# Optimization experiments

Hardware: AMD Instinct MI355X
Metric: run time of the kernel (lower is better)

The kernel has to match this reference:

```python
import jax, jax.numpy as jnp
from jax import lax
import numpy as np

GZ = 15.0   # grid extent (float, from gz=15.0)
G = 15      # grid cells per axis


def _disty(p):
    # p: [B, N, 3] points in [0, GZ). 12 features per point:
    # offsets to cell center / lower corner / upper corner (9) + their euclidean norms (3)
    c = jnp.floor(jnp.clip(p, 0.0, GZ - 1e-4))
    off_c = p - (c + 0.5)
    off_l = p - c
    off_u = p - (c + 1.0)
    norms = jnp.stack([jnp.sqrt((o * o).sum(-1)) for o in (off_c, off_l, off_u)], axis=-1)
    return jnp.concatenate([off_c, off_l, off_u, norms], axis=-1)  # [B, N, 12]


def _mlp(x, W1, b1, W2, b2, W3, b3):
    h = jax.nn.elu(x @ W1 + b1)
    h = jax.nn.elu(h @ W2 + b2)
    return h @ W3 + b3  # [B, N, 4]


def _agg(feats, p):
    # scatter-max per-point features into the [G,G,G] grid of each scene
    B, N, C = feats.shape
    cell = jnp.floor(jnp.clip(p, 0.0, GZ - 1e-4)).astype(jnp.int32)  # [B, N, 3]
    flat = (cell[..., 0] * G + cell[..., 1]) * G + cell[..., 2]
    flat = flat + (jnp.arange(B, dtype=jnp.int32) * (G ** 3))[:, None]
    grid = jnp.zeros((B * G ** 3, C), feats.dtype)
    grid = grid.at[flat.reshape(-1)].max(feats.reshape(-1, C))
    return grid.reshape(B, G, G, G, C).transpose(0, 4, 1, 2, 3)  # [B, 4, G, G, G]


def _conv_bn_elu(x, w, b, g, beta, stride):
    y = lax.conv_general_dilated(x, w, (stride,) * 3, [(2, 2)] * 3,
                                 dimension_numbers=('NCDHW', 'OIDHW', 'NCDHW'))
    y = y + b[None, :, None, None, None]
    # BatchNorm3d, training mode (batch statistics), eps=1e-5
    m = y.mean((0, 2, 3, 4), keepdims=True)
    v = ((y - m) ** 2).mean((0, 2, 3, 4), keepdims=True)
    y = (y - m) * lax.rsqrt(v + 1e-5)
    y = y * g[None, :, None, None, None] + beta[None, :, None, None, None]
    return jax.nn.elu(y)


def setup_inputs():
    key = jax.random.key(0)
    ks = jax.random.split(key, 16)
    B, N = 4, 300000
    pts = lambda k: jax.random.uniform(k, (B, N, 3), jnp.float32, 0.0, GZ)
    lin = lambda k, i, o: (jax.random.normal(k, (i, o), jnp.float32) / np.sqrt(i)).astype(jnp.float32)
    inp = {
        'goals': pts(ks[0]), 'inputs': pts(ks[1]), 'backgrounds': pts(ks[2]),
        'W1': lin(ks[3], 12, 16), 'b1': jnp.zeros((16,), jnp.float32),
        'W2': lin(ks[4], 16, 16), 'b2': jnp.zeros((16,), jnp.float32),
        'W3': lin(ks[5], 16, 4),  'b3': jnp.zeros((4,), jnp.float32),
        'conv1_w': (jax.random.normal(ks[6], (8, 12, 5, 5, 5), jnp.float32) / np.sqrt(12 * 125)).astype(jnp.float32),
        'conv1_b': jnp.zeros((8,), jnp.float32),
        'bn1_g': jnp.ones((8,), jnp.float32), 'bn1_b': jnp.zeros((8,), jnp.float32),
        'convs_w': (jax.random.normal(ks[7], (6, 8, 8, 5, 5, 5), jnp.float32) / np.sqrt(8 * 125)).astype(jnp.float32),
        'convs_b': jnp.zeros((6, 8), jnp.float32),
        'bns_g': jnp.ones((6, 8), jnp.float32), 'bns_b': jnp.zeros((6, 8), jnp.float32),
    }
    return inp


def reference(goals, inputs, backgrounds, W1, b1, W2, b2, W3, b3,
              conv1_w, conv1_b, bn1_g, bn1_b, convs_w, convs_b, bns_g, bns_b):
    def encode(p):
        return _agg(_mlp(_disty(p), W1, b1, W2, b2, W3, b3), p)

    scenes = jnp.concatenate([encode(inputs), encode(goals), encode(backgrounds)], axis=1)  # [B,12,G,G,G]
    x = _conv_bn_elu(scenes, conv1_w, conv1_b, bn1_g, bn1_b, 2)  # [B,8,8,8,8]
    for i in range(6):
        x = _conv_bn_elu(x, convs_w[i], convs_b[i], bns_g[i], bns_b[i], 1)
    return x
```

## Files before the change

kernel.cpp:

```cpp
#include <hip/hip_runtime.h>
#include <math.h>

#define B 4
#define NPTS 300000
#define G 15
#define G3 3375
#define PAIR_FLOATS (4*G3)
#define SCENE_FLOATS (B*12*G3)

typedef float v2f __attribute__((ext_vector_type(2)));

__device__ __forceinline__ float eluf(float v) {
    return v > 0.0f ? v : __expf(v) - 1.0f;
}

__global__ __launch_bounds__(256)
void mlp_kernel(const float* __restrict__ P0,
                const float* __restrict__ P1,
                const float* __restrict__ P2,
                const float* __restrict__ W1, const float* __restrict__ b1,
                const float* __restrict__ W2, const float* __restrict__ b2,
                const float* __restrict__ W3, const float* __restrict__ b3,
                float4* __restrict__ vals, unsigned short* __restrict__ cells,
                float* __restrict__ stats,
                int s0, int m)
{
    if (blockIdx.x == 0 && blockIdx.y == 0 && blockIdx.z == 0 && threadIdx.x < 128)
        stats[threadIdx.x] = 0.0f;

    int b   = blockIdx.y;
    int set = blockIdx.z;
    int i   = blockIdx.x * 256 + threadIdx.x;
    if (i >= m) return;
    const float* P = (set == 0) ? P0 : ((set == 1) ? P1 : P2);

    const float* p = P + ((size_t)b * NPTS + (size_t)(s0 + i)) * 3;
    float px = p[0], py = p[1], pz = p[2];

    const float HI = 14.9999f;
    float cx = floorf(fminf(fmaxf(px, 0.0f), HI));
    float cy = floorf(fminf(fmaxf(py, 0.0f), HI));
    float cz = floorf(fminf(fmaxf(pz, 0.0f), HI));

    float x[12];
    x[0] = px - (cx + 0.5f); x[1] = py - (cy + 0.5f); x[2] = pz - (cz + 0.5f);
    x[3] = px - cx;          x[4] = py - cy;          x[5] = pz - cz;
    x[6] = px - (cx + 1.0f); x[7] = py - (cy + 1.0f); x[8] = pz - (cz + 1.0f);
    x[9]  = sqrtf(x[0]*x[0] + x[1]*x[1] + x[2]*x[2]);
    x[10] = sqrtf(x[3]*x[3] + x[4]*x[4] + x[5]*x[5]);
    x[11] = sqrtf(x[6]*x[6] + x[7]*x[7] + x[8]*x[8]);

    const v2f* W1v = (const v2f*)W1;
    const v2f* W2v = (const v2f*)W2;
    const v2f* W3v = (const v2f*)W3;
    const v2f* b1v = (const v2f*)b1;
    const v2f* b2v = (const v2f*)b2;
    const v2f* b3v = (const v2f*)b3;

    float h1[16];
#pragma unroll
    for (int j2 = 0; j2 < 8; ++j2) {
        v2f s = b1v[j2];
#pragma unroll
        for (int k = 0; k < 12; ++k) {
            v2f xb; xb.x = x[k]; xb.y = x[k];
            s = xb * W1v[k * 8 + j2] + s;
        }
        h1[2*j2]   = eluf(s.x);
        h1[2*j2+1] = eluf(s.y);
    }
    float h2[16];
#pragma unroll
    for (int j2 = 0; j2 < 8; ++j2) {
        v2f s = b2v[j2];
#pragma unroll
        for (int k = 0; k < 16; ++k) {
            v2f xb; xb.x = h1[k]; xb.y = h1[k];
            s = xb * W2v[k * 8 + j2] + s;
        }
        h2[2*j2]   = eluf(s.x);
        h2[2*j2+1] = eluf(s.y);
    }
    v2f o01 = b3v[0], o23 = b3v[1];
#pragma unroll
    for (int k = 0; k < 16; ++k) {
        v2f xb; xb.x = h2[k]; xb.y = h2[k];
        o01 = xb * W3v[k * 2 + 0] + o01;
        o23 = xb * W3v[k * 2 + 1] + o23;
    }

    int cell = (((int)cx) * G + (int)cy) * G + (int)cz;
    int pair = b * 3 + set;
    vals [(size_t)pair * m + i] = make_float4(o01.x, o01.y, o23.x, o23.y);
    cells[(size_t)pair * m + i] = (unsigned short)cell;
}

__global__ __launch_bounds__(512)
void scatter_kernel(const float4* __restrict__ vals,
                    const unsigned short* __restrict__ cells,
                    float* __restrict__ scenesR, int K, int m, int carry)
{
    __shared__ unsigned sg[PAIR_FLOATS];

    int rep = blockIdx.x;
    int b   = blockIdx.y;
    int set = blockIdx.z;
    int pair = b * 3 + set;
    float* myrep = scenesR + ((size_t)pair * K + rep) * PAIR_FLOATS;

    if (carry) {
        for (int i = threadIdx.x; i < PAIR_FLOATS; i += 512)
            sg[i] = __float_as_uint(myrep[i]);
    } else {
        for (int i = threadIdx.x; i < PAIR_FLOATS; i += 512)
            sg[i] = 0u;
    }
    __syncthreads();

    int chunk = (m + K - 1) / K;
    int start = rep * chunk;
    int end   = min(m, start + chunk);
    const float4*         v = vals  + (size_t)pair * m;
    const unsigned short* c = cells + (size_t)pair * m;

    for (int i = start + (int)threadIdx.x; i < end; i += 512) {
        float4 o = v[i];
        int cell = c[i];
        if (o.x > 0.0f) atomicMax(&sg[          cell], __float_as_uint(o.x));
        if (o.y > 0.0f) atomicMax(&sg[    G3 + cell], __float_as_uint(o.y));
        if (o.z > 0.0f) atomicMax(&sg[2 * G3 + cell], __float_as_uint(o.z));
        if (o.w > 0.0f) atomicMax(&sg[3 * G3 + cell], __float_as_uint(o.w));
    }
    __syncthreads();

    for (int i = threadIdx.x; i < PAIR_FLOATS; i += 512)
        myrep[i] = __uint_as_float(sg[i]);
}

__global__ __launch_bounds__(256)
void reduce_kernel(const float* __restrict__ scenesR, float* __restrict__ scenes,
                   int K)
{
    int t = blockIdx.x * 256 + threadIdx.x;
    if (t >= SCENE_FLOATS) return;
    int pair = t / PAIR_FLOATS;
    int j    = t - pair * PAIR_FLOATS;
    const float* src = scenesR + (size_t)pair * K * PAIR_FLOATS + j;
    float mx = 0.0f;
    for (int r = 0; r < K; ++r)
        mx = fmaxf(mx, src[(size_t)r * PAIR_FLOATS]);
    scenes[t] = mx;
}

__global__ __launch_bounds__(768)
void conv1_kernel(const float* __restrict__ scenes,
                  const float* __restrict__ w,
                  const float* __restrict__ bias,
                  float* __restrict__ y, float* __restrict__ stats)
{
    __shared__ float sred[768];
    int bx = blockIdx.x;
    int od = bx & 7, co = (bx >> 3) & 7, b = bx >> 6;
    int tid = threadIdx.x;
    int ow = tid & 7, oh = (tid >> 3) & 7, ci = tid >> 6;

    const float* sc = scenes + (size_t)(b * 12 + ci) * G3;
    const float* wc = w + (size_t)(co * 12 + ci) * 125;
    float s = 0.0f;
#pragma unroll
    for (int kd = 0; kd < 5; ++kd) {
        int id = od * 2 - 2 + kd;
        if ((unsigned)id >= (unsigned)G) continue;
#pragma unroll
        for (int kh = 0; kh < 5; ++kh) {
            int ih = oh * 2 - 2 + kh;
            bool hok = (unsigned)ih < (unsigned)G;
#pragma unroll
            for (int kw = 0; kw < 5; ++kw) {
                int iw = ow * 2 - 2 + kw;
                if (hok && (unsigned)iw < (unsigned)G)
                    s = fmaf(sc[(id * G + ih) * G + iw], wc[kd*25 + kh*5 + kw], s);
            }
        }
    }
    sred[tid] = s;
    __syncthreads();
    if (tid < 64) {
        float tot = bias[co];
#pragma unroll
        for (int g2 = 0; g2 < 12; ++g2) tot += sred[g2 * 64 + tid];
        y[(size_t)(b * 8 + co) * 512 + od * 64 + tid] = tot;
        float sum = tot, sq = tot * tot;
#pragma unroll
        for (int o = 32; o > 0; o >>= 1) {
            sum += __shfl_down(sum, o, 64);
            sq  += __shfl_down(sq,  o, 64);
        }
        if (tid == 0) { atomicAdd(&stats[co], sum); atomicAdd(&stats[8 + co], sq); }
    }
}

__global__ __launch_bounds__(512)
void conv_s_kernel(const float* __restrict__ yin,
                   const float* __restrict__ w,
                   const float* __restrict__ bias,
                   const float* __restrict__ g, const float* __restrict__ bet,
                   const float* __restrict__ stats_in,
                   float* __restrict__ yout, float* __restrict__ stats_out)
{
    __shared__ float slab[8 * 5 * 144];
    __shared__ float sstat[16], sscale[8], sshift[8];
    __shared__ float sred[512];

    int bx = blockIdx.x;
    int od = bx & 7, co = (bx >> 3) & 7, b = bx >> 6;
    int tid = threadIdx.x;

    float raw[8];
#pragma unroll
    for (int k = 0; k < 8; ++k) {
        int r = k * 512 + tid;
        raw[k] = yin[((size_t)(b * 8) << 9) + r];
    }

    if (tid < 16) sstat[tid] = stats_in[tid];
    for (int i = tid; i < 5760; i += 512) slab[i] = 0.0f;
    __syncthreads();

    if (tid < 8) {
        float S = sstat[tid], Q = sstat[8 + tid];
        float m  = S * (1.0f / 2048.0f);
        float vv = Q * (1.0f / 2048.0f) - m * m;
        float rs = rsqrtf(vv + 1e-5f);
        float sc = g[tid] * rs;
        sscale[tid] = sc;
        sshift[tid] = bet[tid] - m * sc;
    }
    __syncthreads();

#pragma unroll
    for (int k = 0; k < 8; ++k) {
        int r  = k * 512 + tid;
        int ci = r >> 9, rem = r & 511;
        int id = rem >> 6, ih = (rem >> 3) & 7, iw = rem & 7;
        int kd = id - od + 2;
        if ((unsigned)kd < 5u) {
            float t = fmaf(raw[k], sscale[ci], sshift[ci]);
            slab[ci * 720 + kd * 144 + (ih + 2) * 12 + (iw + 2)] =
                t > 0.0f ? t : __expf(t) - 1.0f;
        }
    }
    __syncthreads();

    int ow = tid & 7, oh = (tid >> 3) & 7, ci = tid >> 6;
    const float* sl = slab + ci * 720;
    const float* wc = w + (size_t)(co * 8 + ci) * 125;
    float s = 0.0f;
#pragma unroll
    for (int kd = 0; kd < 5; ++kd) {
#pragma unroll
        for (int kh = 0; kh < 5; ++kh) {
            const float* row = sl + kd * 144 + (oh + kh) * 12 + ow;
            const float* wr = wc + kd * 25 + kh * 5;
#pragma unroll
            for (int kw = 0; kw < 5; ++kw) s = fmaf(row[kw], wr[kw], s);
        }
    }
    sred[tid] = s;
    __syncthreads();
    if (tid < 64) {
        float tot = bias[co];
#pragma unroll
        for (int g2 = 0; g2 < 8; ++g2) tot += sred[g2 * 64 + tid];
        yout[(size_t)(b * 8 + co) * 512 + od * 64 + tid] = tot;
        float sum = tot, sq = tot * tot;
#pragma unroll
        for (int o = 32; o > 0; o >>= 1) {
            sum += __shfl_down(sum, o, 64);
            sq  += __shfl_down(sq,  o, 64);
        }
        if (tid == 0) { atomicAdd(&stats_out[co], sum); atomicAdd(&stats_out[8 + co], sq); }
    }
}

__global__ __launch_bounds__(256)
void bn_final_kernel(const float* __restrict__ yin,
                     const float* __restrict__ g, const float* __restrict__ bet,
                     const float* __restrict__ stats_in, float* __restrict__ outp)
{
    int i = blockIdx.x * 256 + threadIdx.x;
    float v = yin[i];
    int c = (i >> 9) & 7;
    float S = stats_in[c], Q = stats_in[8 + c];
    float m  = S * (1.0f / 2048.0f);
    float vv = Q * (1.0f / 2048.0f) - m * m;
    float rs = rsqrtf(vv + 1e-5f);
    float sc = g[c] * rs;
    float sh = bet[c] - m * sc;
    float t = fmaf(v, sc, sh);
    outp[i] = t > 0.0f ? t : __expf(t) - 1.0f;
}

extern "C" void kernel_launch(void* const* d_in, const int* in_sizes, int n_in,
                              void* d_out, int out_size, void* d_ws, size_t ws_size,
                              hipStream_t stream)
{
    const float* goals       = (const float*)d_in[0];
    const float* inputs      = (const float*)d_in[1];
    const float* backgrounds = (const float*)d_in[2];
    const float* W1 = (const float*)d_in[3];
    const float* b1 = (const float*)d_in[4];
    const float* W2 = (const float*)d_in[5];
    const float* b2 = (const float*)d_in[6];
    const float* W3 = (const float*)d_in[7];
    const float* b3 = (const float*)d_in[8];
    const float* conv1_w = (const float*)d_in[9];
    const float* conv1_b = (const float*)d_in[10];
    const float* bn1_g   = (const float*)d_in[11];
    const float* bn1_b   = (const float*)d_in[12];
    const float* convs_w = (const float*)d_in[13];
    const float* convs_b = (const float*)d_in[14];
    const float* bns_g   = (const float*)d_in[15];
    const float* bns_b   = (const float*)d_in[16];

    long ws_floats = (long)(ws_size / 4);
    long fixed = SCENE_FLOATS + 2L * 16384 + 128;
    static const int plans[][2] = {
        {42,1},{42,2},{42,4},{24,4},{21,6},{16,8},{8,12},{4,16},{2,32},{1,64}};
    int K = 1, S = 64;
    for (int pi = 0; pi < 10; ++pi) {
        int pk = plans[pi][0], ps = plans[pi][1];
        long mseg = (NPTS + ps - 1) / ps;
        long need = 54L * mseg + (long)pk * SCENE_FLOATS + fixed;
        if (need <= ws_floats) { K = pk; S = ps; break; }
    }
    int Mseg = (NPTS + S - 1) / S;

    float*          wsp     = (float*)d_ws;
    float4*         vals    = (float4*)wsp;
    unsigned short* cells   = (unsigned short*)(wsp + 48L * Mseg);
    float*          scenesR = wsp + 54L * Mseg;
    float*          scenes  = scenesR + (size_t)K * SCENE_FLOATS;
    float*          yA      = scenes + SCENE_FLOATS;
    float*          yB      = yA + 16384;
    float*          stats   = yB + 16384;

    for (int s = 0; s < S; ++s) {
        int s0 = s * Mseg;
        int m  = min(Mseg, NPTS - s0);
        dim3 agrid((m + 255) / 256, B, 3);
        mlp_kernel<<<agrid, 256, 0, stream>>>(inputs, goals, backgrounds,
                                              W1, b1, W2, b2, W3, b3,
                                              vals, cells, stats, s0, m);
        dim3 bgrid(K, B, 3);
        scatter_kernel<<<bgrid, 512, 0, stream>>>(vals, cells, scenesR, K, m,
                                                  s > 0 ? 1 : 0);
    }

    reduce_kernel<<<(SCENE_FLOATS + 255) / 256, 256, 0, stream>>>(scenesR, scenes, K);

    conv1_kernel<<<256, 768, 0, stream>>>(scenes, conv1_w, conv1_b, yA, stats);

    const float* cur = yA;
    float* nxt = yB;
    for (int i = 0; i < 6; ++i) {
        const float* g   = (i == 0) ? bn1_g : (bns_g + (i - 1) * 8);
        const float* bet = (i == 0) ? bn1_b : (bns_b + (i - 1) * 8);
        conv_s_kernel<<<256, 512, 0, stream>>>(
            cur, convs_w + (size_t)i * 8000, convs_b + i * 8,
            g, bet, stats + i * 16, nxt, stats + (i + 1) * 16);
        const float* tmp = cur; cur = nxt; nxt = (float*)tmp;
    }

    bn_final_kernel<<<64, 256, 0, stream>>>(cur, bns_g + 5 * 8, bns_b + 5 * 8,
                                            stats + 6 * 16, (float*)d_out);
}
```

Baseline: 279.7 us.

## Merge scatter replicas with global atomicMax and fuse final BN into last conv

The per-replica scene buffers and the separate reduce kernel are removed. Each scatter block now merges its shared-memory grid directly into a single global scene buffer with atomicMax, and that buffer is zeroed inside the first MLP launch. The standalone BN/ELU epilogue kernel is folded into the last conv_s launch using a last-block-done counter with coherent loads. This cuts two kernel launches and the replica write/read traffic, but adds global atomic contention and depends on relaxed-atomic ordering for correctness.

```diff
diff --git a/kernel.cpp b/kernel.cpp
--- a/kernel.cpp
+++ b/kernel.cpp
@@ -7,11 +7,20 @@
 #define G3 3375
 #define PAIR_FLOATS (4*G3)
 #define SCENE_FLOATS (B*12*G3)
+#define RCHUNKS 42
 
 typedef float v2f __attribute__((ext_vector_type(2)));
 
 __device__ __forceinline__ float eluf(float v) {
     return v > 0.0f ? v : __expf(v) - 1.0f;
+}
+
+__device__ __forceinline__ float coh_load(const float* p) {
+    return __hip_atomic_fetch_add((float*)p, 0.0f, __ATOMIC_RELAXED,
+                                  __HIP_MEMORY_SCOPE_AGENT);
+}
+__device__ __forceinline__ void coh_store(float* p, float v) {
+    __hip_atomic_exchange(p, v, __ATOMIC_RELAXED, __HIP_MEMORY_SCOPE_AGENT);
 }
 
 __global__ __launch_bounds__(256)
@@ -22,11 +31,18 @@
                 const float* __restrict__ W2, const float* __restrict__ b2,
                 const float* __restrict__ W3, const float* __restrict__ b3,
                 float4* __restrict__ vals, unsigned short* __restrict__ cells,
-                float* __restrict__ stats,
+                float* __restrict__ stats, float* __restrict__ scenes,
                 int s0, int m)
 {
-    if (blockIdx.x == 0 && blockIdx.y == 0 && blockIdx.z == 0 && threadIdx.x < 128)
-        stats[threadIdx.x] = 0.0f;
+    if (s0 == 0) {
+        if (blockIdx.x == 0 && blockIdx.y == 0 && blockIdx.z == 0 &&
+            threadIdx.x < 128)
+            stats[threadIdx.x] = 0.0f;
+        if (blockIdx.y == 0 && blockIdx.z == 0) {
+            int t = blockIdx.x * 256 + threadIdx.x;
+            if (t < SCENE_FLOATS) scenes[t] = 0.0f;
+        }
+    }
 
     int b   = blockIdx.y;
     int set = blockIdx.z;
@@ -98,7 +114,7 @@
 __global__ __launch_bounds__(512)
 void scatter_kernel(const float4* __restrict__ vals,
                     const unsigned short* __restrict__ cells,
-                    float* __restrict__ scenesR, int K, int m, int carry)
+                    float* __restrict__ scenes, int m)
 {
     __shared__ unsigned sg[PAIR_FLOATS];
 
@@ -106,18 +122,11 @@
     int b   = blockIdx.y;
     int set = blockIdx.z;
     int pair = b * 3 + set;
-    float* myrep = scenesR + ((size_t)pair * K + rep) * PAIR_FLOATS;
-
-    if (carry) {
-        for (int i = threadIdx.x; i < PAIR_FLOATS; i += 512)
-            sg[i] = __float_as_uint(myrep[i]);
-    } else {
-        for (int i = threadIdx.x; i < PAIR_FLOATS; i += 512)
-            sg[i] = 0u;
-    }
-    __syncthreads();
-
-    int chunk = (m + K - 1) / K;
+
+    for (int i = threadIdx.x; i < PAIR_FLOATS; i += 512) sg[i] = 0u;
+    __syncthreads();
+
+    int chunk = (m + RCHUNKS - 1) / RCHUNKS;
     int start = rep * chunk;
     int end   = min(m, start + chunk);
     const float4*         v = vals  + (size_t)pair * m;
@@ -133,23 +142,11 @@
     }
     __syncthreads();
 
-    for (int i = threadIdx.x; i < PAIR_FLOATS; i += 512)
-        myrep[i] = __uint_as_float(sg[i]);
-}
-
-__global__ __launch_bounds__(256)
-void reduce_kernel(const float* __restrict__ scenesR, float* __restrict__ scenes,
-                   int K)
-{
-    int t = blockIdx.x * 256 + threadIdx.x;
-    if (t >= SCENE_FLOATS) return;
-    int pair = t / PAIR_FLOATS;
-    int j    = t - pair * PAIR_FLOATS;
-    const float* src = scenesR + (size_t)pair * K * PAIR_FLOATS + j;
-    float mx = 0.0f;
-    for (int r = 0; r < K; ++r)
-        mx = fmaxf(mx, src[(size_t)r * PAIR_FLOATS]);
-    scenes[t] = mx;
+    unsigned* dst = (unsigned*)scenes + (size_t)pair * PAIR_FLOATS;
+    for (int i = threadIdx.x; i < PAIR_FLOATS; i += 512) {
+        unsigned u = sg[i];
+        if (u) atomicMax(dst + i, u);
+    }
 }
 
 __global__ __launch_bounds__(768)
@@ -206,7 +203,10 @@
                    const float* __restrict__ bias,
                    const float* __restrict__ g, const float* __restrict__ bet,
                    const float* __restrict__ stats_in,
-                   float* __restrict__ yout, float* __restrict__ stats_out)
+                   float* __restrict__ yout, float* __restrict__ stats_out,
+                   const float* __restrict__ gN, const float* __restrict__ betN,
+                   unsigned* __restrict__ cnt, float* __restrict__ outp,
+                   int last)
 {
     __shared__ float slab[8 * 5 * 144];
     __shared__ float sstat[16], sscale[8], sshift[8];
@@ -272,7 +272,9 @@
         float tot = bias[co];
 #pragma unroll
         for (int g2 = 0; g2 < 8; ++g2) tot += sred[g2 * 64 + tid];
-        yout[(size_t)(b * 8 + co) * 512 + od * 64 + tid] = tot;
+        size_t oidx = ((size_t)(b * 8 + co) << 9) + od * 64 + tid;
+        if (last) coh_store(yout + oidx, tot);
+        else      yout[oidx] = tot;
         float sum = tot, sq = tot * tot;
 #pragma unroll
         for (int o = 32; o > 0; o >>= 1) {
@@ -281,24 +283,37 @@
         }
         if (tid == 0) { atomicAdd(&stats_out[co], sum); atomicAdd(&stats_out[8 + co], sq); }
     }
-}
-
-__global__ __launch_bounds__(256)
-void bn_final_kernel(const float* __restrict__ yin,
-                     const float* __restrict__ g, const float* __restrict__ bet,
-                     const float* __restrict__ stats_in, float* __restrict__ outp)
-{
-    int i = blockIdx.x * 256 + threadIdx.x;
-    float v = yin[i];
-    int c = (i >> 9) & 7;
-    float S = stats_in[c], Q = stats_in[8 + c];
-    float m  = S * (1.0f / 2048.0f);
-    float vv = Q * (1.0f / 2048.0f) - m * m;
-    float rs = rsqrtf(vv + 1e-5f);
-    float sc = g[c] * rs;
-    float sh = bet[c] - m * sc;
-    float t = fmaf(v, sc, sh);
-    outp[i] = t > 0.0f ? t : __expf(t) - 1.0f;
+
+    if (!last) return;
+
+    __syncthreads();
+    __shared__ unsigned amLast;
+    if (tid == 0) {
+        unsigned old = __hip_atomic_fetch_add(cnt, 1u, __ATOMIC_RELAXED,
+                                              __HIP_MEMORY_SCOPE_AGENT);
+        amLast = (old == 255u) ? 1u : 0u;
+    }
+    __syncthreads();
+    if (!amLast) return;
+
+    __shared__ float fsc[8], fsh[8];
+    if (tid < 8) {
+        float S = coh_load(stats_out + tid);
+        float Q = coh_load(stats_out + 8 + tid);
+        float mm = S * (1.0f / 2048.0f);
+        float vv = Q * (1.0f / 2048.0f) - mm * mm;
+        float rs = rsqrtf(vv + 1e-5f);
+        float sc2 = gN[tid] * rs;
+        fsc[tid] = sc2;
+        fsh[tid] = betN[tid] - mm * sc2;
+    }
+    __syncthreads();
+    for (int i2 = tid; i2 < 16384; i2 += 512) {
+        float v = coh_load(yout + i2);
+        int c = (i2 >> 9) & 7;
+        float t = fmaf(v, fsc[c], fsh[c]);
+        outp[i2] = t > 0.0f ? t : __expf(t) - 1.0f;
+    }
 }
 
 extern "C" void kernel_launch(void* const* d_in, const int* in_sizes, int n_in,
@@ -325,25 +340,21 @@
 
     long ws_floats = (long)(ws_size / 4);
     long fixed = SCENE_FLOATS + 2L * 16384 + 128;
-    static const int plans[][2] = {
-        {42,1},{42,2},{42,4},{24,4},{21,6},{16,8},{8,12},{4,16},{2,32},{1,64}};
-    int K = 1, S = 64;
-    for (int pi = 0; pi < 10; ++pi) {
-        int pk = plans[pi][0], ps = plans[pi][1];
+    int S = 64;
+    for (int ps = 1; ps <= 64; ps *= 2) {
         long mseg = (NPTS + ps - 1) / ps;
-        long need = 54L * mseg + (long)pk * SCENE_FLOATS + fixed;
-        if (need <= ws_floats) { K = pk; S = ps; break; }
+        if (54L * mseg + fixed <= ws_floats) { S = ps; break; }
     }
     int Mseg = (NPTS + S - 1) / S;
 
     float*          wsp     = (float*)d_ws;
     float4*         vals    = (float4*)wsp;
     unsigned short* cells   = (unsigned short*)(wsp + 48L * Mseg);
-    float*          scenesR = wsp + 54L * Mseg;
-    float*          scenes  = scenesR + (size_t)K * SCENE_FLOATS;
+    float*          scenes  = wsp + 54L * Mseg;
     float*          yA      = scenes + SCENE_FLOATS;
     float*          yB      = yA + 16384;
     float*          stats   = yB + 16384;
+    unsigned*       cnt     = (unsigned*)(stats + 116);
 
     for (int s = 0; s < S; ++s) {
         int s0 = s * Mseg;
@@ -351,13 +362,10 @@
         dim3 agrid((m + 255) / 256, B, 3);
         mlp_kernel<<<agrid, 256, 0, stream>>>(inputs, goals, backgrounds,
                                               W1, b1, W2, b2, W3, b3,
-                                              vals, cells, stats, s0, m);
-        dim3 bgrid(K, B, 3);
-        scatter_kernel<<<bgrid, 512, 0, stream>>>(vals, cells, scenesR, K, m,
-                                                  s > 0 ? 1 : 0);
-    }
-
-    reduce_kernel<<<(SCENE_FLOATS + 255) / 256, 256, 0, stream>>>(scenesR, scenes, K);
+                                              vals, cells, stats, scenes, s0, m);
+        dim3 bgrid(RCHUNKS, B, 3);
+        scatter_kernel<<<bgrid, 512, 0, stream>>>(vals, cells, scenes, m);
+    }
 
     conv1_kernel<<<256, 768, 0, stream>>>(scenes, conv1_w, conv1_b, yA, stats);
 
@@ -368,10 +376,9 @@
         const float* bet = (i == 0) ? bn1_b : (bns_b + (i - 1) * 8);
         conv_s_kernel<<<256, 512, 0, stream>>>(
             cur, convs_w + (size_t)i * 8000, convs_b + i * 8,
-            g, bet, stats + i * 16, nxt, stats + (i + 1) * 16);
+            g, bet, stats + i * 16, nxt, stats + (i + 1) * 16,
+            bns_g + 5 * 8, bns_b + 5 * 8, cnt, (float*)d_out,
+            (i == 5) ? 1 : 0);
         const float* tmp = cur; cur = nxt; nxt = (float*)tmp;
     }
-
-    bn_final_kernel<<<64, 256, 0, stream>>>(cur, bns_g + 5 * 8, bns_b + 5 * 8,
-                                            stats + 6 * 16, (float*)d_out);
-}
+}
```

Measured after the change: 287.4 us. +2.8%, slower.
